# Optimization experiments

Hardware: AMD Instinct MI355X
Metric: run time of the kernel (lower is better)

Reference implementation:

```python
import jax, jax.numpy as jnp
import numpy as np

# dims
B, D_IN, HID, G, K = 64, 5000, 1000, 512, 8
N_LABELS, GROUP_SIZE, M = 262144, 512, 32
C = K * GROUP_SIZE  # candidates per sample after topk group expansion


def setup_inputs() -> dict:
    key = jax.random.key(0)
    ks = jax.random.split(key, 8)
    x = jax.random.normal(ks[0], (B, D_IN), jnp.float32)
    candidates = jax.random.randint(ks[1], (B, M), 0, N_LABELS, dtype=jnp.int32)
    labels = (jax.random.uniform(ks[2], (B, M)) < 0.2).astype(jnp.float32)
    group_labels = (jax.random.uniform(ks[3], (B, G)) < 0.05).astype(jnp.float32)
    W1 = jax.random.normal(ks[4], (HID, D_IN), jnp.float32) * 0.02
    b1 = jnp.zeros((HID,), jnp.float32)
    W2 = jax.random.normal(ks[5], (G, HID), jnp.float32) * 0.02
    b2 = jnp.zeros((G,), jnp.float32)
    emb = jax.random.normal(ks[6], (N_LABELS, G), jnp.float32) * 0.02
    # equal-size contiguous groups (makes the torch pad-to-max a no-op)
    group_y = jnp.arange(N_LABELS, dtype=jnp.int32).reshape(G, GROUP_SIZE)
    return dict(x=x, candidates=candidates, labels=labels, group_labels=group_labels,
                W1=W1, b1=b1, W2=W2, b2=b2, emb=emb, group_y=group_y)


def _bce_with_logits(z, t):
    # mean over all elements of log(1+e^z) - z*t (stable)
    return jnp.mean(jnp.logaddexp(0.0, z) - z * t)


def reference(x, candidates, labels, group_labels, W1, b1, W2, b2, emb, group_y):
    # router MLP: Linear -> ReLU -> Linear -> sigmoid
    h = jax.nn.relu(x @ W1.T + b1)                 # [B, HID]
    y = jax.nn.sigmoid(h @ W2.T + b2)              # [B, G]
    # topk group select on detached scores
    _, idx = jax.lax.top_k(jax.lax.stop_gradient(y), K)   # [B, K]
    cand = group_y[idx].reshape(B, C)              # [B, C] gathered candidate label ids
    # build per-candidate binary targets: candidate is positive iff it appears
    # among the masked ground-truth candidates of that sample
    tgt = jnp.where(labels > 0.5, candidates, -1)  # [B, M]
    new_labels = (cand[:, :, None] == tgt[:, None, :]).any(-1).astype(jnp.float32)  # [B, C]
    # gathered embedding bmm scoring
    ew = emb[cand]                                 # [B, C, G]
    logits = jnp.einsum('bcg,bg->bc', ew, y)       # [B, C]
    loss = _bce_with_logits(logits, new_labels) + _bce_with_logits(y, group_labels)
    return logits, loss
```

## Files before the change

kernel.cpp:

```cpp
#include <hip/hip_runtime.h>
#include <math.h>

static constexpr int BB  = 64;
static constexpr int DIN = 5000;
static constexpr int NHID = 1000;
static constexpr int NG  = 512;
static constexpr int NK  = 8;
static constexpr int NM  = 32;
static constexpr int GS  = 512;
static constexpr int NC  = NK * GS;

static constexpr int S1 = 16, CHD1 = 320, IT1 = 16, IP1 = 1024;
static constexpr int S2 = 16, CHD2 = 64,  IT2 = 8,  IP2 = 512;

__global__ __launch_bounds__(256) void gemm64(
    const float* __restrict__ A, int lda,
    const float* __restrict__ Bm, int ldb, int Ireal,
    float* __restrict__ part, int Ipad, int Itiles, int D, int CHD)
{
  __shared__ __align__(16) float xT[32][64];
  __shared__ __align__(16) float wT[32][64];
  const int tid = threadIdx.x;
  const int itile = blockIdx.x % Itiles;
  const int s = blockIdx.x / Itiles;
  const int d_beg = s * CHD;
  const int d_end = min(D, d_beg + CHD);
  const int tx = tid & 15;
  const int ty = tid >> 4;
  float acc[4][4] = {};

  for (int d0 = d_beg; d0 < d_end; d0 += 32) {
#pragma unroll
    for (int q = 0; q < 2; q++) {
      int lin = q * 256 + tid;
      int r = lin >> 3;
      int c4 = (lin & 7) << 2;
      int d = d0 + c4;
      const float* pr = A + (size_t)r * lda;
      float4 v = make_float4(0.f, 0.f, 0.f, 0.f);
      if (d + 4 <= d_end) v = *(const float4*)(pr + d);
      else {
        if (d + 0 < d_end) v.x = pr[d + 0];
        if (d + 1 < d_end) v.y = pr[d + 1];
        if (d + 2 < d_end) v.z = pr[d + 2];
        if (d + 3 < d_end) v.w = pr[d + 3];
      }
      xT[c4 + 0][r] = v.x; xT[c4 + 1][r] = v.y;
      xT[c4 + 2][r] = v.z; xT[c4 + 3][r] = v.w;
    }
#pragma unroll
    for (int q = 0; q < 2; q++) {
      int lin = q * 256 + tid;
      int r = lin >> 3;
      int c4 = (lin & 7) << 2;
      int ib = itile * 64 + r;
      int d = d0 + c4;
      float4 v = make_float4(0.f, 0.f, 0.f, 0.f);
      if (ib < Ireal) {
        const float* pr = Bm + (size_t)ib * ldb;
        if (d + 4 <= d_end) v = *(const float4*)(pr + d);
        else {
          if (d + 0 < d_end) v.x = pr[d + 0];
          if (d + 1 < d_end) v.y = pr[d + 1];
          if (d + 2 < d_end) v.z = pr[d + 2];
          if (d + 3 < d_end) v.w = pr[d + 3];
        }
      }
      wT[c4 + 0][r] = v.x; wT[c4 + 1][r] = v.y;
      wT[c4 + 2][r] = v.z; wT[c4 + 3][r] = v.w;
    }
    __syncthreads();
    const int nn = min(32, d_end - d0);
    if (nn == 32) {
#pragma unroll
      for (int dd = 0; dd < 32; dd++) {
        float4 xv = *(const float4*)&xT[dd][tx << 2];
        float4 wv = *(const float4*)&wT[dd][ty << 2];
        float xr[4] = {xv.x, xv.y, xv.z, xv.w};
        float wr[4] = {wv.x, wv.y, wv.z, wv.w};
#pragma unroll
        for (int a = 0; a < 4; a++)
#pragma unroll
          for (int c = 0; c < 4; c++)
            acc[a][c] = fmaf(xr[a], wr[c], acc[a][c]);
      }
    } else {
      for (int dd = 0; dd < nn; dd++) {
        float4 xv = *(const float4*)&xT[dd][tx << 2];
        float4 wv = *(const float4*)&wT[dd][ty << 2];
        float xr[4] = {xv.x, xv.y, xv.z, xv.w};
        float wr[4] = {wv.x, wv.y, wv.z, wv.w};
#pragma unroll
        for (int a = 0; a < 4; a++)
#pragma unroll
          for (int c = 0; c < 4; c++)
            acc[a][c] = fmaf(xr[a], wr[c], acc[a][c]);
      }
    }
    __syncthreads();
  }

  const int b0 = tx << 2;
  const int i0 = itile * 64 + (ty << 2);
#pragma unroll
  for (int a = 0; a < 4; a++) {
    float4 vv = make_float4(acc[a][0], acc[a][1], acc[a][2], acc[a][3]);
    *(float4*)&part[((size_t)s * BB + (b0 + a)) * Ipad + i0] = vv;
  }
}

__global__ void reduce_act(const float* __restrict__ part, int S, int Ipad, int Ireal,
                           const float* __restrict__ bias, float* __restrict__ out,
                           int ostride, int mode)
{
  int lin = blockIdx.x * blockDim.x + threadIdx.x;
  int n = BB * Ireal;
  if (lin >= n) return;
  int b = lin / Ireal;
  int i = lin - b * Ireal;
  float sum = bias[i];
  for (int s = 0; s < S; s++) sum += part[((size_t)s * BB + b) * Ipad + i];
  if (mode == 0) sum = fmaxf(sum, 0.f);
  else           sum = 1.f / (1.f + expf(-sum));
  out[(size_t)b * ostride + i] = sum;
}

__global__ __launch_bounds__(64) void topk_loss2(
    const float* __restrict__ y, const float* __restrict__ gl,
    int* __restrict__ idxo, float* __restrict__ acc)
{
  const int b = blockIdx.x;
  const int lane = threadIdx.x;
  float v[8];
  float l2 = 0.f;
#pragma unroll
  for (int j = 0; j < 8; j++) {
    int pos = j * 64 + lane;
    float z = y[b * NG + pos];
    v[j] = z;
    float t = gl[b * NG + pos];
    l2 += fmaxf(z, 0.f) + log1pf(expf(-fabsf(z))) - z * t;
  }
  for (int k = 0; k < 8; k++) {
    float bv = -INFINITY;
    int bi = 0x7fffffff;
#pragma unroll
    for (int j = 0; j < 8; j++) {
      int pos = j * 64 + lane;
      if (v[j] > bv) { bv = v[j]; bi = pos; }
    }
#pragma unroll
    for (int off = 32; off >= 1; off >>= 1) {
      float ov = __shfl_xor(bv, off, 64);
      int   oi = __shfl_xor(bi, off, 64);
      if (ov > bv || (ov == bv && oi < bi)) { bv = ov; bi = oi; }
    }
    if (lane == 0) idxo[b * NK + k] = bi;
    if (lane == (bi & 63)) {
      int jj = bi >> 6;
#pragma unroll
      for (int j = 0; j < 8; j++) if (j == jj) v[j] = -INFINITY;
    }
  }
#pragma unroll
  for (int off = 32; off >= 1; off >>= 1) l2 += __shfl_xor(l2, off, 64);
  if (lane == 0) atomicAdd(acc + 1, l2);
}

__global__ __launch_bounds__(512) void score_kernel(
    const float* __restrict__ emb, const float* __restrict__ y,
    const int* __restrict__ idxb, const int* __restrict__ cands,
    const float* __restrict__ labels, const int* __restrict__ group_y,
    float* __restrict__ out, float* __restrict__ acc)
{
  const int bx = blockIdx.x;
  const int b = bx >> 3;
  const int k = bx & 7;
  __shared__ __align__(16) float yl[NG];
  __shared__ int cid[GS];
  __shared__ int tgt[NM];
  __shared__ float red[8];
  const int tid = threadIdx.x;
  const int g = idxb[b * NK + k];
  yl[tid] = y[b * NG + tid];
  cid[tid] = group_y[g * GS + tid];
  if (tid < NM) tgt[tid] = labels[b * NM + tid] > 0.5f ? cands[b * NM + tid] : -1;
  __syncthreads();

  const int l = tid & 15;
  const int grp = tid >> 4;
  const float4* yl4 = (const float4*)yl;
  float lossp = 0.f;

  for (int it = 0; it < 16; it++) {
    int row = it * 32 + grp;
    int r = cid[row];
    const float4* ep = (const float4*)(emb + (size_t)r * NG);
    float sum = 0.f;
#pragma unroll
    for (int seg = 0; seg < 8; seg++) {
      float4 e  = ep[seg * 16 + l];
      float4 yv = yl4[seg * 16 + l];
      sum = fmaf(e.x, yv.x, sum);
      sum = fmaf(e.y, yv.y, sum);
      sum = fmaf(e.z, yv.z, sum);
      sum = fmaf(e.w, yv.w, sum);
    }
    sum += __shfl_xor(sum, 1, 64);
    sum += __shfl_xor(sum, 2, 64);
    sum += __shfl_xor(sum, 4, 64);
    sum += __shfl_xor(sum, 8, 64);
    if (l == 0) {
      out[((size_t)b * NK + k) * GS + row] = sum;
      float nl = 0.f;
#pragma unroll
      for (int m = 0; m < NM; m++) if (r == tgt[m]) nl = 1.f;
      lossp += fmaxf(sum, 0.f) + log1pf(expf(-fabsf(sum))) - sum * nl;
    }
  }
#pragma unroll
  for (int off = 32; off >= 1; off >>= 1) lossp += __shfl_xor(lossp, off, 64);
  const int wid = tid >> 6;
  if ((tid & 63) == 0) red[wid] = lossp;
  __syncthreads();
  if (tid == 0) {
    float t = 0.f;
#pragma unroll
    for (int w = 0; w < 8; w++) t += red[w];
    atomicAdd(acc, t);
  }
}

__global__ void finalize_loss(const float* __restrict__ acc, float* __restrict__ out)
{
  out[(size_t)BB * NC] = acc[0] * (1.f / (float)(BB * NC)) +
                         acc[1] * (1.f / (float)(BB * NG));
}

extern "C" void kernel_launch(void* const* d_in, const int* in_sizes, int n_in,
                              void* d_out, int out_size, void* d_ws, size_t ws_size,
                              hipStream_t stream)
{
  const float* x      = (const float*)d_in[0];
  const int*   cands  = (const int*)  d_in[1];
  const float* labels = (const float*)d_in[2];
  const float* glab   = (const float*)d_in[3];
  const float* W1     = (const float*)d_in[4];
  const float* b1     = (const float*)d_in[5];
  const float* W2     = (const float*)d_in[6];
  const float* b2     = (const float*)d_in[7];
  const float* emb    = (const float*)d_in[8];
  const int*   gy     = (const int*)  d_in[9];
  float* out = (float*)d_out;

  float* ws   = (float*)d_ws;
  float* acc  = ws;
  float* y    = ws + 16;
  int*   idxb = (int*)(y + BB * NG);
  float* h    = (float*)(idxb + 512);
  float* p1   = h + (size_t)BB * IP1;
  float* p2   = p1 + (size_t)S1 * BB * IP1;

  hipMemsetAsync(acc, 0, 2 * sizeof(float), stream);

  gemm64<<<IT1 * S1, 256, 0, stream>>>(x, DIN, W1, DIN, NHID, p1, IP1, IT1, DIN, CHD1);
  reduce_act<<<(BB * NHID + 255) / 256, 256, 0, stream>>>(p1, S1, IP1, NHID, b1, h, IP1, 0);

  gemm64<<<IT2 * S2, 256, 0, stream>>>(h, IP1, W2, NHID, NG, p2, IP2, IT2, NHID, CHD2);
  reduce_act<<<(BB * NG + 255) / 256, 256, 0, stream>>>(p2, S2, IP2, NG, b2, y, NG, 1);

  topk_loss2<<<BB, 64, 0, stream>>>(y, glab, idxb, acc);

  score_kernel<<<BB * NK, 512, 0, stream>>>(emb, y, idxb, cands, labels, gy, out, acc);

  finalize_loss<<<1, 1, 0, stream>>>(acc, out);
}
```

Baseline: 143.0 us.

## Deduplicate selected groups so each embedding block is gathered once per unique group

A new single-block kernel finds the unique groups among all (sample, k) top-k selections and lists the pairs that chose each group. The scoring kernel then launches one block per unique group. Each block loads every embedding row into registers once and reuses it for up to eight samples' y vectors staged in shared memory. The aim is to cut redundant gathers from the large embedding table, at the cost of an extra serial O(n^2) prep kernel and possible load imbalance across blocks with different pair counts.

```diff
diff --git a/kernel.cpp b/kernel.cpp
--- a/kernel.cpp
+++ b/kernel.cpp
@@ -9,6 +9,7 @@
 static constexpr int NM  = 32;
 static constexpr int GS  = 512;
 static constexpr int NC  = NK * GS;
+static constexpr int NPAIR = BB * NK;
 
 static constexpr int S1 = 16, CHD1 = 320, IT1 = 16, IP1 = 1024;
 static constexpr int S2 = 16, CHD2 = 64,  IT2 = 8,  IP2 = 512;
@@ -167,57 +168,113 @@
   if (lane == 0) atomicAdd(acc + 1, l2);
 }
 
-__global__ __launch_bounds__(512) void score_kernel(
+__global__ __launch_bounds__(512) void prep_groups(
+    const int* __restrict__ idxb, int* __restrict__ ug, int* __restrict__ ucnt,
+    int* __restrict__ upairs, int* __restrict__ ucountp)
+{
+  __shared__ int gs[NPAIR];
+  __shared__ int fs[NPAIR];
+  const int i = threadIdx.x;
+  gs[i] = idxb[i];
+  __syncthreads();
+  const int g = gs[i];
+  int first = i, rank = 0, cnt = 0;
+  for (int j = 0; j < NPAIR; j++) {
+    int gj = gs[j];
+    if (gj == g) { cnt++; if (j < first) first = j; if (j < i) rank++; }
+  }
+  fs[i] = first;
+  __syncthreads();
+  int uid = 0;
+  for (int j = 0; j < first; j++) uid += (fs[j] == j);
+  if (first == i) { ug[uid] = g; ucnt[uid] = cnt; }
+  upairs[uid * 64 + rank] = i;
+  if (i == 0) {
+    int total = 0;
+    for (int j = 0; j < NPAIR; j++) total += (fs[j] == j);
+    *ucountp = total;
+  }
+}
+
+__global__ __launch_bounds__(512) void score2(
     const float* __restrict__ emb, const float* __restrict__ y,
-    const int* __restrict__ idxb, const int* __restrict__ cands,
-    const float* __restrict__ labels, const int* __restrict__ group_y,
-    float* __restrict__ out, float* __restrict__ acc)
-{
-  const int bx = blockIdx.x;
-  const int b = bx >> 3;
-  const int k = bx & 7;
-  __shared__ __align__(16) float yl[NG];
+    const int* __restrict__ ug, const int* __restrict__ ucnt,
+    const int* __restrict__ upairs, const int* __restrict__ ucountp,
+    const int* __restrict__ cands, const float* __restrict__ labels,
+    const int* __restrict__ group_y, float* __restrict__ out,
+    float* __restrict__ acc)
+{
+  const int j = blockIdx.x;
+  if (j >= *ucountp) return;
+  const int g = ug[j];
+  const int P = ucnt[j];
   __shared__ int cid[GS];
-  __shared__ int tgt[NM];
+  __shared__ int plist[64];
+  __shared__ __align__(16) float yl[8][NG];
+  __shared__ int tgtc[8][NM];
   __shared__ float red[8];
   const int tid = threadIdx.x;
-  const int g = idxb[b * NK + k];
-  yl[tid] = y[b * NG + tid];
   cid[tid] = group_y[g * GS + tid];
-  if (tid < NM) tgt[tid] = labels[b * NM + tid] > 0.5f ? cands[b * NM + tid] : -1;
-  __syncthreads();
+  if (tid < P) plist[tid] = upairs[j * 64 + tid];
 
   const int l = tid & 15;
   const int grp = tid >> 4;
-  const float4* yl4 = (const float4*)yl;
   float lossp = 0.f;
 
-  for (int it = 0; it < 16; it++) {
-    int row = it * 32 + grp;
-    int r = cid[row];
-    const float4* ep = (const float4*)(emb + (size_t)r * NG);
-    float sum = 0.f;
-#pragma unroll
-    for (int seg = 0; seg < 8; seg++) {
-      float4 e  = ep[seg * 16 + l];
-      float4 yv = yl4[seg * 16 + l];
-      sum = fmaf(e.x, yv.x, sum);
-      sum = fmaf(e.y, yv.y, sum);
-      sum = fmaf(e.z, yv.z, sum);
-      sum = fmaf(e.w, yv.w, sum);
-    }
-    sum += __shfl_xor(sum, 1, 64);
-    sum += __shfl_xor(sum, 2, 64);
-    sum += __shfl_xor(sum, 4, 64);
-    sum += __shfl_xor(sum, 8, 64);
-    if (l == 0) {
-      out[((size_t)b * NK + k) * GS + row] = sum;
-      float nl = 0.f;
-#pragma unroll
-      for (int m = 0; m < NM; m++) if (r == tgt[m]) nl = 1.f;
-      lossp += fmaxf(sum, 0.f) + log1pf(expf(-fabsf(sum))) - sum * nl;
-    }
-  }
+  for (int c0 = 0; c0 < P; c0 += 8) {
+    const int pc = min(8, P - c0);
+    __syncthreads();
+    {
+      int p = tid >> 6;
+      int e = (tid & 63) * 8;
+      if (p < pc) {
+        int b = plist[c0 + p] >> 3;
+        const float4* src = (const float4*)(y + (size_t)b * NG + e);
+        float4* dst = (float4*)&yl[p][e];
+        dst[0] = src[0]; dst[1] = src[1];
+      }
+      if (tid < pc * NM) {
+        int pp = tid >> 5, m = tid & 31;
+        int b = plist[c0 + pp] >> 3;
+        tgtc[pp][m] = labels[b * NM + m] > 0.5f ? cands[b * NM + m] : -1;
+      }
+    }
+    __syncthreads();
+
+    for (int it = 0; it < 16; it++) {
+      int row = it * 32 + grp;
+      int r = cid[row];
+      const float4* ep = (const float4*)(emb + (size_t)r * NG);
+      float4 e[8];
+#pragma unroll
+      for (int seg = 0; seg < 8; seg++) e[seg] = ep[seg * 16 + l];
+      for (int p = 0; p < pc; p++) {
+        const float4* yp4 = (const float4*)yl[p];
+        float sum = 0.f;
+#pragma unroll
+        for (int seg = 0; seg < 8; seg++) {
+          float4 yv = yp4[seg * 16 + l];
+          sum = fmaf(e[seg].x, yv.x, sum);
+          sum = fmaf(e[seg].y, yv.y, sum);
+          sum = fmaf(e[seg].z, yv.z, sum);
+          sum = fmaf(e[seg].w, yv.w, sum);
+        }
+        sum += __shfl_xor(sum, 1, 64);
+        sum += __shfl_xor(sum, 2, 64);
+        sum += __shfl_xor(sum, 4, 64);
+        sum += __shfl_xor(sum, 8, 64);
+        if (l == 0) {
+          int pair = plist[c0 + p];
+          out[(size_t)pair * GS + row] = sum;
+          float nl = 0.f;
+#pragma unroll
+          for (int m = 0; m < NM; m++) if (r == tgtc[p][m]) nl = 1.f;
+          lossp += fmaxf(sum, 0.f) + log1pf(expf(-fabsf(sum))) - sum * nl;
+        }
+      }
+    }
+  }
+
 #pragma unroll
   for (int off = 32; off >= 1; off >>= 1) lossp += __shfl_xor(lossp, off, 64);
   const int wid = tid >> 6;
@@ -257,9 +314,13 @@
   float* acc  = ws;
   float* y    = ws + 16;
   int*   idxb = (int*)(y + BB * NG);
-  float* h    = (float*)(idxb + 512);
+  float* h    = (float*)(idxb + NPAIR);
   float* p1   = h + (size_t)BB * IP1;
   float* p2   = p1 + (size_t)S1 * BB * IP1;
+  int*   ug   = (int*)(p2 + (size_t)S2 * BB * IP2);
+  int*   ucnt = ug + NPAIR;
+  int*   ucountp = ucnt + NPAIR;
+  int*   upairs  = ucountp + 16;
 
   hipMemsetAsync(acc, 0, 2 * sizeof(float), stream);
 
@@ -271,7 +332,10 @@
 
   topk_loss2<<<BB, 64, 0, stream>>>(y, glab, idxb, acc);
 
-  score_kernel<<<BB * NK, 512, 0, stream>>>(emb, y, idxb, cands, labels, gy, out, acc);
+  prep_groups<<<1, NPAIR, 0, stream>>>(idxb, ug, ucnt, upairs, ucountp);
+
+  score2<<<NPAIR, 512, 0, stream>>>(emb, y, ug, ucnt, upairs, ucountp,
+                                    cands, labels, gy, out, acc);
 
   finalize_loss<<<1, 1, 0, stream>>>(acc, out);
 }
```

Result: slower. 523.0 us (+265.7%).

## Sort (sample,group) pairs by group and split score blocks for L2 reuse

Applied to the files above, without the earlier changes.

Adds a single-block rank sort that orders the 512 (sample, topk-slot) pairs by selected group id. The scoring kernel is split into two half-group blocks per pair and remapped so blocks sharing the same group are scheduled near each other. This targets better cache reuse of embedding rows, since many samples pick the same groups, and doubles block count for more parallelism. It costs an extra kernel launch plus an O(N^2) shared-memory sort.

```diff
diff --git a/kernel.cpp b/kernel.cpp
--- a/kernel.cpp
+++ b/kernel.cpp
@@ -9,6 +9,7 @@
 static constexpr int NM  = 32;
 static constexpr int GS  = 512;
 static constexpr int NC  = NK * GS;
+static constexpr int NPAIR = BB * NK;
 
 static constexpr int S1 = 16, CHD1 = 320, IT1 = 16, IP1 = 1024;
 static constexpr int S2 = 16, CHD2 = 64,  IT2 = 8,  IP2 = 512;
@@ -167,24 +168,45 @@
   if (lane == 0) atomicAdd(acc + 1, l2);
 }
 
-__global__ __launch_bounds__(512) void score_kernel(
+__global__ __launch_bounds__(512) void sort_pairs(
+    const int* __restrict__ idxb, int* __restrict__ order)
+{
+  __shared__ int gs[NPAIR];
+  const int i = threadIdx.x;
+  gs[i] = idxb[i];
+  __syncthreads();
+  const int g = gs[i];
+  int pos = 0;
+  for (int j = 0; j < NPAIR; j++) {
+    int gj = gs[j];
+    pos += (gj < g) || (gj == g && j < i);
+  }
+  order[pos] = i;
+}
+
+__global__ __launch_bounds__(512) void score3(
     const float* __restrict__ emb, const float* __restrict__ y,
-    const int* __restrict__ idxb, const int* __restrict__ cands,
-    const float* __restrict__ labels, const int* __restrict__ group_y,
-    float* __restrict__ out, float* __restrict__ acc)
-{
-  const int bx = blockIdx.x;
-  const int b = bx >> 3;
-  const int k = bx & 7;
+    const int* __restrict__ order, const int* __restrict__ idxb,
+    const int* __restrict__ cands, const float* __restrict__ labels,
+    const int* __restrict__ group_y, float* __restrict__ out,
+    float* __restrict__ acc)
+{
+  const int L = (blockIdx.x & 7) * 128 + (blockIdx.x >> 3);
+  const int pair = order[L >> 1];
+  const int half = L & 1;
+  const int b = pair >> 3;
+  const int g = idxb[pair];
   __shared__ __align__(16) float yl[NG];
-  __shared__ int cid[GS];
+  __shared__ int cid[256];
   __shared__ int tgt[NM];
   __shared__ float red[8];
   const int tid = threadIdx.x;
-  const int g = idxb[b * NK + k];
   yl[tid] = y[b * NG + tid];
-  cid[tid] = group_y[g * GS + tid];
-  if (tid < NM) tgt[tid] = labels[b * NM + tid] > 0.5f ? cands[b * NM + tid] : -1;
+  if (tid < 256) cid[tid] = group_y[g * GS + half * 256 + tid];
+  if (tid >= 256 && tid < 256 + NM) {
+    int m = tid - 256;
+    tgt[m] = labels[b * NM + m] > 0.5f ? cands[b * NM + m] : -1;
+  }
   __syncthreads();
 
   const int l = tid & 15;
@@ -192,9 +214,10 @@
   const float4* yl4 = (const float4*)yl;
   float lossp = 0.f;
 
-  for (int it = 0; it < 16; it++) {
-    int row = it * 32 + grp;
-    int r = cid[row];
+  for (int it = 0; it < 8; it++) {
+    int rloc = it * 32 + grp;
+    int row = half * 256 + rloc;
+    int r = cid[rloc];
     const float4* ep = (const float4*)(emb + (size_t)r * NG);
     float sum = 0.f;
 #pragma unroll
@@ -211,7 +234,7 @@
     sum += __shfl_xor(sum, 4, 64);
     sum += __shfl_xor(sum, 8, 64);
     if (l == 0) {
-      out[((size_t)b * NK + k) * GS + row] = sum;
+      out[(size_t)pair * GS + row] = sum;
       float nl = 0.f;
 #pragma unroll
       for (int m = 0; m < NM; m++) if (r == tgt[m]) nl = 1.f;
@@ -257,9 +280,10 @@
   float* acc  = ws;
   float* y    = ws + 16;
   int*   idxb = (int*)(y + BB * NG);
-  float* h    = (float*)(idxb + 512);
+  float* h    = (float*)(idxb + NPAIR);
   float* p1   = h + (size_t)BB * IP1;
   float* p2   = p1 + (size_t)S1 * BB * IP1;
+  int*   order = (int*)(p2 + (size_t)S2 * BB * IP2);
 
   hipMemsetAsync(acc, 0, 2 * sizeof(float), stream);
 
@@ -271,7 +295,9 @@
 
   topk_loss2<<<BB, 64, 0, stream>>>(y, glab, idxb, acc);
 
-  score_kernel<<<BB * NK, 512, 0, stream>>>(emb, y, idxb, cands, labels, gy, out, acc);
+  sort_pairs<<<1, NPAIR, 0, stream>>>(idxb, order);
+
+  score3<<<2 * NPAIR, 512, 0, stream>>>(emb, y, order, idxb, cands, labels, gy, out, acc);
 
   finalize_loss<<<1, 1, 0, stream>>>(acc, out);
 }
```

New measurement: 125.0 us (median of 2 runs). -12.6%, faster.

## Group (sample,group) pairs by selected group to reuse embedding rows across samples

Applied to the files above, without the earlier changes.

The per-sample top-k kernel becomes a single 512-thread block that also sorts all (batch,k) pairs by selected group and builds segments of up to 8 pairs that share a group. The scoring kernel then loads each 64-row embedding slice once into registers and dots it against up to 8 samples' y vectors, cutting redundant emb reads when many samples pick the same groups. Separately, the first GEMM's split-K changes from 16 to 23 chunks. The cost is a serial single-block prep kernel with O(512^2) rank computation, plus many early-exiting blocks in a fixed 4096-block launch.

```diff
diff --git a/kernel.cpp b/kernel.cpp
--- a/kernel.cpp
+++ b/kernel.cpp
@@ -9,8 +9,9 @@
 static constexpr int NM  = 32;
 static constexpr int GS  = 512;
 static constexpr int NC  = NK * GS;
-
-static constexpr int S1 = 16, CHD1 = 320, IT1 = 16, IP1 = 1024;
+static constexpr int NPAIR = BB * NK;
+
+static constexpr int S1 = 23, CHD1 = 224, IT1 = 16, IP1 = 1024;
 static constexpr int S2 = 16, CHD2 = 64,  IT2 = 8,  IP2 = 512;
 
 __global__ __launch_bounds__(256) void gemm64(
@@ -125,110 +126,161 @@
   out[(size_t)b * ostride + i] = sum;
 }
 
-__global__ __launch_bounds__(64) void topk_loss2(
+__global__ __launch_bounds__(512) void prep512(
     const float* __restrict__ y, const float* __restrict__ gl,
-    int* __restrict__ idxo, float* __restrict__ acc)
-{
-  const int b = blockIdx.x;
-  const int lane = threadIdx.x;
-  float v[8];
+    int* __restrict__ order, int* __restrict__ sg, int* __restrict__ sstart,
+    int* __restrict__ scnt, int* __restrict__ Sn, float* __restrict__ acc)
+{
+  __shared__ int gs[NPAIR];
+  __shared__ int flag[NPAIR];
+  const int tid = threadIdx.x;
+  const int w = tid >> 6, lane = tid & 63;
+
   float l2 = 0.f;
-#pragma unroll
-  for (int j = 0; j < 8; j++) {
-    int pos = j * 64 + lane;
-    float z = y[b * NG + pos];
-    v[j] = z;
-    float t = gl[b * NG + pos];
-    l2 += fmaxf(z, 0.f) + log1pf(expf(-fabsf(z))) - z * t;
-  }
-  for (int k = 0; k < 8; k++) {
-    float bv = -INFINITY;
-    int bi = 0x7fffffff;
+  for (int bs = 0; bs < 8; bs++) {
+    const int b = w * 8 + bs;
+    float v[8];
 #pragma unroll
     for (int j = 0; j < 8; j++) {
       int pos = j * 64 + lane;
-      if (v[j] > bv) { bv = v[j]; bi = pos; }
-    }
-#pragma unroll
-    for (int off = 32; off >= 1; off >>= 1) {
-      float ov = __shfl_xor(bv, off, 64);
-      int   oi = __shfl_xor(bi, off, 64);
-      if (ov > bv || (ov == bv && oi < bi)) { bv = ov; bi = oi; }
-    }
-    if (lane == 0) idxo[b * NK + k] = bi;
-    if (lane == (bi & 63)) {
-      int jj = bi >> 6;
-#pragma unroll
-      for (int j = 0; j < 8; j++) if (j == jj) v[j] = -INFINITY;
+      float z = y[b * NG + pos];
+      v[j] = z;
+      float t = gl[b * NG + pos];
+      l2 += fmaxf(z, 0.f) + log1pf(expf(-fabsf(z))) - z * t;
+    }
+    for (int k = 0; k < 8; k++) {
+      float bv = -INFINITY;
+      int bi = 0x7fffffff;
+#pragma unroll
+      for (int j = 0; j < 8; j++) {
+        int pos = j * 64 + lane;
+        if (v[j] > bv) { bv = v[j]; bi = pos; }
+      }
+#pragma unroll
+      for (int off = 32; off >= 1; off >>= 1) {
+        float ov = __shfl_xor(bv, off, 64);
+        int   oi = __shfl_xor(bi, off, 64);
+        if (ov > bv || (ov == bv && oi < bi)) { bv = ov; bi = oi; }
+      }
+      if (lane == 0) gs[b * NK + k] = bi;
+      if (lane == (bi & 63)) {
+        int jj = bi >> 6;
+#pragma unroll
+        for (int j = 0; j < 8; j++) if (j == jj) v[j] = -INFINITY;
+      }
     }
   }
 #pragma unroll
   for (int off = 32; off >= 1; off >>= 1) l2 += __shfl_xor(l2, off, 64);
   if (lane == 0) atomicAdd(acc + 1, l2);
-}
-
-__global__ __launch_bounds__(512) void score_kernel(
+  __syncthreads();
+
+  const int i = tid;
+  const int g = gs[i];
+  int pos = 0, first = 0, m = 0;
+  for (int j = 0; j < NPAIR; j++) {
+    int gj = gs[j];
+    int lt = (gj < g);
+    pos += lt | ((gj == g) & (j < i));
+    first += lt;
+    m += (gj == g);
+  }
+  const int runpos = pos - first;
+  const int isS = ((runpos & 7) == 0) ? 1 : 0;
+  flag[pos] = isS;
+  order[pos] = i;
+  __syncthreads();
+  int slot = 0;
+  for (int p = 0; p < pos; p++) slot += flag[p];
+  if (isS) {
+    sg[slot] = g;
+    sstart[slot] = pos;
+    scnt[slot] = min(8, m - runpos);
+  }
+  if (pos == NPAIR - 1) Sn[0] = slot + isS;
+}
+
+__global__ __launch_bounds__(256) void score5(
     const float* __restrict__ emb, const float* __restrict__ y,
-    const int* __restrict__ idxb, const int* __restrict__ cands,
+    const int* __restrict__ order, const int* __restrict__ sg,
+    const int* __restrict__ sstart, const int* __restrict__ scnt,
+    const int* __restrict__ Sn, const int* __restrict__ cands,
     const float* __restrict__ labels, const int* __restrict__ group_y,
     float* __restrict__ out, float* __restrict__ acc)
 {
-  const int bx = blockIdx.x;
-  const int b = bx >> 3;
-  const int k = bx & 7;
-  __shared__ __align__(16) float yl[NG];
-  __shared__ int cid[GS];
-  __shared__ int tgt[NM];
-  __shared__ float red[8];
+  const int S_n = Sn[0];
+  const int T = S_n * 8;
+  const int Q = (T + 7) >> 3;
+  const int c = blockIdx.x & 7;
+  const int r = blockIdx.x >> 3;
+  if (r >= Q) return;
+  const int L = c * Q + r;
+  if (L >= T) return;
+  const int s = L >> 3, e8 = L & 7;
+  const int g = sg[s], pc = scnt[s], base = sstart[s];
+
+  __shared__ __align__(16) float yl[8][NG];
+  __shared__ int cid[64];
+  __shared__ int plist[8];
+  __shared__ int tgt[8][NM];
+  __shared__ float red[4];
   const int tid = threadIdx.x;
-  const int g = idxb[b * NK + k];
-  yl[tid] = y[b * NG + tid];
-  cid[tid] = group_y[g * GS + tid];
-  if (tid < NM) tgt[tid] = labels[b * NM + tid] > 0.5f ? cands[b * NM + tid] : -1;
-  __syncthreads();
-
-  const int l = tid & 15;
-  const int grp = tid >> 4;
-  const float4* yl4 = (const float4*)yl;
+  if (tid < 8 && tid < pc) plist[tid] = order[base + tid];
+  if (tid >= 64 && tid < 128) cid[tid - 64] = group_y[g * GS + e8 * 64 + (tid - 64)];
+  __syncthreads();
+  {
+    int p = tid >> 5, j = tid & 31;
+    if (p < pc) {
+      int b = plist[p] >> 3;
+      const float4* src = (const float4*)(y + (size_t)b * NG);
+      float4* dst = (float4*)yl[p];
+      dst[j] = src[j]; dst[j + 32] = src[j + 32];
+      dst[j + 64] = src[j + 64]; dst[j + 96] = src[j + 96];
+      tgt[p][j] = labels[b * NM + j] > 0.5f ? cands[b * NM + j] : -1;
+    }
+  }
+  __syncthreads();
+
+  const int l = tid & 15, lg = tid >> 4;
   float lossp = 0.f;
-
-  for (int it = 0; it < 16; it++) {
-    int row = it * 32 + grp;
-    int r = cid[row];
-    const float4* ep = (const float4*)(emb + (size_t)r * NG);
-    float sum = 0.f;
-#pragma unroll
-    for (int seg = 0; seg < 8; seg++) {
-      float4 e  = ep[seg * 16 + l];
-      float4 yv = yl4[seg * 16 + l];
-      sum = fmaf(e.x, yv.x, sum);
-      sum = fmaf(e.y, yv.y, sum);
-      sum = fmaf(e.z, yv.z, sum);
-      sum = fmaf(e.w, yv.w, sum);
-    }
-    sum += __shfl_xor(sum, 1, 64);
-    sum += __shfl_xor(sum, 2, 64);
-    sum += __shfl_xor(sum, 4, 64);
-    sum += __shfl_xor(sum, 8, 64);
-    if (l == 0) {
-      out[((size_t)b * NK + k) * GS + row] = sum;
-      float nl = 0.f;
-#pragma unroll
-      for (int m = 0; m < NM; m++) if (r == tgt[m]) nl = 1.f;
-      lossp += fmaxf(sum, 0.f) + log1pf(expf(-fabsf(sum))) - sum * nl;
+  for (int it = 0; it < 4; it++) {
+    const int rloc = it * 16 + lg;
+    const int row = e8 * 64 + rloc;
+    const int rid = cid[rloc];
+    const float4* ep = (const float4*)(emb + (size_t)rid * NG);
+    float4 e[8];
+#pragma unroll
+    for (int seg = 0; seg < 8; seg++) e[seg] = ep[seg * 16 + l];
+    for (int p = 0; p < pc; p++) {
+      const float4* yp = (const float4*)yl[p];
+      float sum = 0.f;
+#pragma unroll
+      for (int seg = 0; seg < 8; seg++) {
+        float4 yv = yp[seg * 16 + l];
+        sum = fmaf(e[seg].x, yv.x, sum);
+        sum = fmaf(e[seg].y, yv.y, sum);
+        sum = fmaf(e[seg].z, yv.z, sum);
+        sum = fmaf(e[seg].w, yv.w, sum);
+      }
+      sum += __shfl_xor(sum, 1, 64);
+      sum += __shfl_xor(sum, 2, 64);
+      sum += __shfl_xor(sum, 4, 64);
+      sum += __shfl_xor(sum, 8, 64);
+      if (l == 0) {
+        int pair = plist[p];
+        out[(size_t)pair * GS + row] = sum;
+        float nl = 0.f;
+#pragma unroll
+        for (int mm = 0; mm < NM; mm++) if (rid == tgt[p][mm]) nl = 1.f;
+        lossp += fmaxf(sum, 0.f) + log1pf(expf(-fabsf(sum))) - sum * nl;
+      }
     }
   }
 #pragma unroll
   for (int off = 32; off >= 1; off >>= 1) lossp += __shfl_xor(lossp, off, 64);
-  const int wid = tid >> 6;
-  if ((tid & 63) == 0) red[wid] = lossp;
-  __syncthreads();
-  if (tid == 0) {
-    float t = 0.f;
-#pragma unroll
-    for (int w = 0; w < 8; w++) t += red[w];
-    atomicAdd(acc, t);
-  }
+  if ((tid & 63) == 0) red[tid >> 6] = lossp;
+  __syncthreads();
+  if (tid == 0) atomicAdd(acc, red[0] + red[1] + red[2] + red[3]);
 }
 
 __global__ void finalize_loss(const float* __restrict__ acc, float* __restrict__ out)
@@ -256,10 +308,14 @@
   float* ws   = (float*)d_ws;
   float* acc  = ws;
   float* y    = ws + 16;
-  int*   idxb = (int*)(y + BB * NG);
-  float* h    = (float*)(idxb + 512);
+  float* h    = y + BB * NG;
   float* p1   = h + (size_t)BB * IP1;
   float* p2   = p1 + (size_t)S1 * BB * IP1;
+  int* order  = (int*)(p2 + (size_t)S2 * BB * IP2);
+  int* sg     = order + NPAIR;
+  int* sstart = sg + NPAIR;
+  int* scnt   = sstart + NPAIR;
+  int* Sn     = scnt + NPAIR;
 
   hipMemsetAsync(acc, 0, 2 * sizeof(float), stream);
 
@@ -269,9 +325,10 @@
   gemm64<<<IT2 * S2, 256, 0, stream>>>(h, IP1, W2, NHID, NG, p2, IP2, IT2, NHID, CHD2);
   reduce_act<<<(BB * NG + 255) / 256, 256, 0, stream>>>(p2, S2, IP2, NG, b2, y, NG, 1);
 
-  topk_loss2<<<BB, 64, 0, stream>>>(y, glab, idxb, acc);
-
-  score_kernel<<<BB * NK, 512, 0, stream>>>(emb, y, idxb, cands, labels, gy, out, acc);
+  prep512<<<1, NPAIR, 0, stream>>>(y, glab, order, sg, sstart, scnt, Sn, acc);
+
+  score5<<<4096, 256, 0, stream>>>(emb, y, order, sg, sstart, scnt, Sn,
+                                   cands, labels, gy, out, acc);
 
   finalize_loss<<<1, 1, 0, stream>>>(acc, out);
 }
```

Measured after the change: 218.9 us. 53.0% more time.
